# Kernel optimization log

Hardware: AMD Instinct MI355X
Metric: run time of the kernel (lower is better)

The kernel has to match this reference:

```python
import jax, jax.numpy as jnp
import numpy as np

# Config constants (match init_kwargs)
E = 16          # n_routed_experts
G = 4           # n_groups
TOPK_G = 2      # topk_groups
K = 4           # n_activated_experts
ROUTE_SCALE = 2.5446


def setup_inputs() -> dict:
    key = jax.random.key(0)
    ks = jax.random.split(key, 9)
    T, D, H = 2048, 1024, 704
    HS = 2 * H  # shared FFN hidden = n_shared_experts * expert_hidden_dim
    sc = lambda k, shape, fan_in: (jax.random.normal(k, shape, jnp.float32)
                                   * (fan_in ** -0.5))
    return {
        "x":      jax.random.normal(ks[0], (T, D), jnp.float32),
        "gate_w": sc(ks[1], (E, D), D),
        "gate_b": jnp.zeros((E,), jnp.float32),       # V3 routing bias (init 0)
        "w1":     sc(ks[2], (E, H, D), D),            # gate proj per expert
        "w3":     sc(ks[3], (E, H, D), D),            # up proj per expert
        "w2":     sc(ks[4], (E, D, H), H),            # down proj per expert
        "ws1":    sc(ks[5], (HS, D), D),              # shared FFN gate proj
        "ws3":    sc(ks[6], (HS, D), D),              # shared FFN up proj
        "ws2":    sc(ks[7], (D, HS), HS),             # shared FFN down proj
    }


def _gate(x, gate_w, gate_b):
    """DeepSeek-V3 sigmoid gate with bias routing + group-limited masking."""
    T = x.shape[0]
    logits = x @ gate_w.T                                   # [T, E]
    scores = jax.nn.sigmoid(logits).astype(jnp.float32)     # original_scores
    routing = scores + gate_b                               # bias only affects routing
    g = routing.reshape(T, G, E // G)
    # use_bias=True -> group score = sum of top-2 routing scores in group
    group_scores = jnp.sum(jax.lax.top_k(g, 2)[0], axis=-1)     # [T, G]
    top_groups = jax.lax.top_k(group_scores, TOPK_G)[1]         # [T, TOPK_G]
    keep = jnp.any(jnp.arange(G)[None, :, None] == top_groups[:, None, :],
                   axis=-1)                                     # [T, G]
    routing = jnp.where(keep[:, :, None], g, -jnp.inf).reshape(T, E)
    idx = jax.lax.top_k(routing, K)[1]                          # [T, K]
    w = jnp.take_along_axis(scores, idx, axis=1)                # un-biased weights
    w = w / jnp.clip(jnp.sum(w, axis=-1, keepdims=True), 1e-9)  # sigmoid renorm
    w = (w * ROUTE_SCALE).astype(x.dtype)
    return w, idx


def reference(x, gate_w, gate_b, w1, w3, w2, ws1, ws3, ws2):
    T, D = x.shape
    weights, idx = _gate(x, gate_w, gate_b)                 # [T,K], [T,K]
    # Dense dispatch/combine matrix: combine[t, e] = gate weight (0 if unrouted)
    combine = jnp.zeros((T, E), x.dtype).at[
        jnp.arange(T)[:, None], idx].add(weights)           # [T, E]
    # Routed experts: SwiGLU per expert, grouped GEMMs
    hg = jnp.einsum('td,ehd->eth', x, w1)                   # [E, T, H]
    hu = jnp.einsum('td,ehd->eth', x, w3)                   # [E, T, H]
    eo = jnp.einsum('eth,edh->etd', jax.nn.silu(hg) * hu, w2)  # [E, T, D]
    y_routed = jnp.einsum('etd,te->td', eo, combine)        # [T, D]
    # Shared experts (always active SwiGLU)
    y_shared = (jax.nn.silu(x @ ws1.T) * (x @ ws3.T)) @ ws2.T
    return y_routed + y_shared
```

## Files before the change

### kernel.cpp

```cpp
#include <hip/hip_runtime.h>
#include <hip/hip_bf16.h>
#include <math.h>

typedef __attribute__((ext_vector_type(4))) float   f32x4;
typedef __attribute__((ext_vector_type(8))) short   short8;
typedef __attribute__((ext_vector_type(8))) __bf16  bf16x8;

union SB8 { short8 s; bf16x8 b; };

__device__ __forceinline__ short f2bf(float f) {
  union { float f; unsigned u; } v; v.f = f;
  unsigned r = v.u + 0x7fffu + ((v.u >> 16) & 1u);
  return (short)(r >> 16);
}

__device__ __forceinline__ short8 cvt8(f32x4 a, f32x4 b) {
  short8 r;
  r[0] = f2bf(a[0]); r[1] = f2bf(a[1]); r[2] = f2bf(a[2]); r[3] = f2bf(a[3]);
  r[4] = f2bf(b[0]); r[5] = f2bf(b[1]); r[6] = f2bf(b[2]); r[7] = f2bf(b[3]);
  return r;
}

__device__ __forceinline__ void ldsload16(const short* g, short* l) {
  __builtin_amdgcn_global_load_lds(
      (const __attribute__((address_space(1))) unsigned int*)g,
      (__attribute__((address_space(3))) unsigned int*)l, 16, 0, 0);
}

#define TT   2048
#define DD   1024
#define HH   704
#define HSS  1408
#define EE   16
#define CAP  2048
#define CSTR 32

#define O1  2097152ULL
#define O2  13631488ULL
#define O3  25165824ULL
#define O4  36700160ULL
#define O5  38141952ULL
#define O6  39583744ULL
#define CVT_TOTAL 41025536ULL

#define W2SZ    11534336ULL
#define WS1SZ   1441792ULL
#define WS1END  26607616ULL
#define CVTA_TOTAL  28049408ULL
#define CVTA_BLOCKS 3424
#define GATE_BLOCKS 512

__global__ __launch_bounds__(256)
void gate_cvt(const float* __restrict__ x,  const float* __restrict__ w1,
              const float* __restrict__ w3, const float* __restrict__ s1,
              const float* __restrict__ s3, short* __restrict__ dst,
              const float* __restrict__ gw, const float* __restrict__ gb,
              int* __restrict__ counts, int* __restrict__ tok,
              float* __restrict__ wgt, int* __restrict__ eslot)
{
  if (blockIdx.x >= GATE_BLOCKS) {
    const int tid = threadIdx.x;
    const size_t base = (size_t)(blockIdx.x - GATE_BLOCKS) * 8192;
    const float* sp[4]; short* dp[4];
    #pragma unroll
    for (int k = 0; k < 4; k++) {
      const size_t sb = base + (size_t)k * 2048;
      const float* src; size_t doff;
      if      (sb < O1)     { src = x  + sb;            doff = sb; }
      else if (sb < O2)     { src = w1 + (sb - O1);     doff = sb; }
      else if (sb < O3)     { src = w3 + (sb - O2);     doff = sb; }
      else if (sb < WS1END) { src = s1 + (sb - O3);     doff = sb + W2SZ; }
      else                  { src = s3 + (sb - WS1END); doff = sb + W2SZ; }
      sp[k] = src + tid * 8;
      dp[k] = dst + doff + tid * 8;
    }
    f32x4 va[8];
    #pragma unroll
    for (int k = 0; k < 4; k++) {
      va[2 * k]     = *(const f32x4*)(sp[k]);
      va[2 * k + 1] = *(const f32x4*)(sp[k] + 4);
    }
    #pragma unroll
    for (int k = 0; k < 4; k++)
      *(short8*)(dp[k]) = cvt8(va[2 * k], va[2 * k + 1]);
    return;
  }

  const int lane = threadIdx.x & 63;
  const int wid  = threadIdx.x >> 6;
  const int t    = blockIdx.x * 4 + wid;
  const int e    = lane & 15;
  const int p    = lane >> 4;

  const float* xp = x + (size_t)t * DD + p * 256;
  const float* gp = gw + (size_t)e * DD + p * 256;

  double a0 = 0.0, a1 = 0.0, a2 = 0.0, a3 = 0.0;
  #pragma unroll 8
  for (int i = 0; i < 64; i++) {
    f32x4 xa = *(const f32x4*)(xp + i * 4);
    f32x4 ga = *(const f32x4*)(gp + i * 4);
    a0 += (double)xa[0] * (double)ga[0];
    a1 += (double)xa[1] * (double)ga[1];
    a2 += (double)xa[2] * (double)ga[2];
    a3 += (double)xa[3] * (double)ga[3];
  }
  double acc = (a0 + a1) + (a2 + a3);
  acc += __shfl_xor(acc, 16);
  acc += __shfl_xor(acc, 32);
  float accf = (float)acc;

  float lf[EE], sc[EE], r[EE];
  #pragma unroll
  for (int j = 0; j < EE; j++) lf[j] = __shfl(accf, j);
  #pragma unroll
  for (int j = 0; j < EE; j++) {
    sc[j] = 1.f / (1.f + expf(-lf[j]));
    r[j] = sc[j] + gb[j];
  }
  float gs[4];
  #pragma unroll
  for (int g = 0; g < 4; g++) {
    float m1 = -1e30f, m2 = -1e30f;
    #pragma unroll
    for (int j = 0; j < 4; j++) {
      float v = r[g * 4 + j];
      if (v > m1) { m2 = m1; m1 = v; }
      else if (v > m2) { m2 = v; }
    }
    gs[g] = m1 + m2;
  }
  int g1 = 0, g2 = -1; float b1 = -1e30f, b2 = -1e30f;
  #pragma unroll
  for (int g = 0; g < 4; g++) {
    if (gs[g] > b1) { b2 = b1; g2 = g1; b1 = gs[g]; g1 = g; }
    else if (gs[g] > b2) { b2 = gs[g]; g2 = g; }
  }
  int idx[4]; float wv[4]; float wsum = 0.f;
  unsigned used = 0;
  #pragma unroll
  for (int k = 0; k < 4; k++) {
    float best = -1e30f; int bi = 0;
    #pragma unroll
    for (int j = 0; j < EE; j++) {
      int g = j >> 2;
      bool keep = (g == g1) || (g == g2);
      if (keep && !((used >> j) & 1) && r[j] > best) { best = r[j]; bi = j; }
    }
    used |= 1u << bi; idx[k] = bi; wv[k] = sc[bi]; wsum += sc[bi];
  }
  float div = wsum < 1e-9f ? 1e-9f : wsum;
  if (lane < 4) {
    float w = wv[lane] / div * 2.5446f;
    int slot = atomicAdd(&counts[idx[lane] * CSTR], 1);
    tok[idx[lane] * CAP + slot] = t;
    wgt[idx[lane] * CAP + slot] = w;
    eslot[t * 4 + lane] = (idx[lane] << 16) | slot;
  }
}

__global__ __launch_bounds__(256, 2)
void gemm1_merged(const short* __restrict__ xb, const short* __restrict__ w1b,
                  const short* __restrict__ w3b, const short* __restrict__ ws1b,
                  const short* __restrict__ ws3b, short* __restrict__ act_r,
                  short* __restrict__ act_s, const int* __restrict__ counts,
                  const int* __restrict__ tok,
                  const float* __restrict__ w2f, const float* __restrict__ ws2f,
                  short* __restrict__ w2bd, short* __restrict__ ws2bd)
{
  const int z = blockIdx.z;
  const int Mt = blockIdx.y, Nt = blockIdx.x;

  if (z == 0) {
    const int bid = Mt * 11 + Nt;
    const int tid = threadIdx.x;
    for (int s = 0; s < 9; s++) {
      const size_t base = (size_t)bid * 73728 + (size_t)s * 8192;
      const float* sp[4]; short* dp[4];
      #pragma unroll
      for (int k = 0; k < 4; k++) {
        const size_t sb = base + (size_t)k * 2048;
        if (sb < W2SZ) {
          sp[k] = w2f + sb + tid * 8;
          dp[k] = w2bd + sb + tid * 8;
        } else {
          const size_t o = sb - W2SZ;
          sp[k] = ws2f + o + tid * 8;
          dp[k] = ws2bd + o + tid * 8;
        }
      }
      f32x4 va[8];
      #pragma unroll
      for (int k = 0; k < 4; k++) {
        va[2 * k]     = *(const f32x4*)(sp[k]);
        va[2 * k + 1] = *(const f32x4*)(sp[k] + 4);
      }
      #pragma unroll
      for (int k = 0; k < 4; k++)
        *(short8*)(dp[k]) = cvt8(va[2 * k], va[2 * k + 1]);
    }
    return;
  }

  const bool routed = (z <= EE);
  const int e = z - 1;

  int cnt, N, rowbase = 0;
  const short *W1, *W3;
  short* act;
  if (routed) {
    if (Nt >= 6) return;
    cnt = counts[e * CSTR];
    if (Mt * 128 >= cnt) return;
    int rb = 0;
    for (int i = 0; i < e; i++) rb += counts[i * CSTR];
    rowbase = rb;
    N = HH;
    W1 = w1b + (size_t)e * HH * DD;
    W3 = w3b + (size_t)e * HH * DD;
    act = act_r;
  } else {
    cnt = TT; N = HSS; W1 = ws1b; W3 = ws3b; act = act_s;
  }

  __shared__ __align__(16) short lA[128 * 64];
  __shared__ __align__(16) short lB1[128 * 64];
  __shared__ __align__(16) short lB3[128 * 64];

  const int tid = threadIdx.x, lane = tid & 63, wv = tid >> 6;
  const int srow = lane >> 3, schunk = lane & 7, scg = schunk ^ srow;

  const short* pa[4]; const short* pb1[4]; const short* pb3[4];
  #pragma unroll
  for (int i = 0; i < 4; i++) {
    const int g = wv * 4 + i;
    int arow = Mt * 128 + g * 8 + srow;
    if (routed) {
      int slot = arow < cnt ? arow : cnt - 1;
      arow = tok[e * CAP + slot];
    }
    pa[i] = xb + (size_t)arow * DD + scg * 8;
    const int brow = Nt * 128 + g * 8 + srow;
    pb1[i] = W1 + (size_t)brow * DD + scg * 8;
    pb3[i] = W3 + (size_t)brow * DD + scg * 8;
  }

  f32x4 acc1[8][2], acc3[8][2];
  #pragma unroll
  for (int i = 0; i < 8; i++) {
    #pragma unroll
    for (int j = 0; j < 2; j++) { acc1[i][j] = (f32x4)0.f; acc3[i][j] = (f32x4)0.f; }
  }

  const int q = lane >> 4, r7 = lane & 7, hi = (lane & 15) >> 3;

  for (int kk = 0; kk < DD; kk += 64) {
    #pragma unroll
    for (int i = 0; i < 4; i++) {
      const int g = wv * 4 + i;
      ldsload16(pa[i] + kk,  lA  + g * 512);
      ldsload16(pb1[i] + kk, lB1 + g * 512);
      ldsload16(pb3[i] + kk, lB3 + g * 512);
    }
    __syncthreads();
    #pragma unroll
    for (int kc = 0; kc < 2; kc++) {
      const int cx = (kc * 4 + q) ^ r7;
      SB8 b1f[2], b3f[2];
      #pragma unroll
      for (int ntl = 0; ntl < 2; ntl++) {
        const int a16 = ((wv * 2 + ntl) * 2 + hi) * 64 + r7 * 8 + cx;
        b1f[ntl].s = *(const short8*)(lB1 + a16 * 8);
        b3f[ntl].s = *(const short8*)(lB3 + a16 * 8);
      }
      #pragma unroll
      for (int mt = 0; mt < 8; mt++) {
        const int a16 = (2 * mt + hi) * 64 + r7 * 8 + cx;
        SB8 af; af.s = *(const short8*)(lA + a16 * 8);
        acc1[mt][0] = __builtin_amdgcn_mfma_f32_16x16x32_bf16(af.b, b1f[0].b, acc1[mt][0], 0, 0, 0);
        acc1[mt][1] = __builtin_amdgcn_mfma_f32_16x16x32_bf16(af.b, b1f[1].b, acc1[mt][1], 0, 0, 0);
        acc3[mt][0] = __builtin_amdgcn_mfma_f32_16x16x32_bf16(af.b, b3f[0].b, acc3[mt][0], 0, 0, 0);
        acc3[mt][1] = __builtin_amdgcn_mfma_f32_16x16x32_bf16(af.b, b3f[1].b, acc3[mt][1], 0, 0, 0);
      }
    }
    __syncthreads();
  }

  const int quad = lane >> 4, lcol = lane & 15;
  #pragma unroll
  for (int mt = 0; mt < 8; mt++) {
    #pragma unroll
    for (int ntl = 0; ntl < 2; ntl++) {
      const int col = Nt * 128 + (wv * 2 + ntl) * 16 + lcol;
      #pragma unroll
      for (int rg = 0; rg < 4; rg++) {
        const int r = Mt * 128 + mt * 16 + quad * 4 + rg;
        if (r < cnt && col < N) {
          float g = acc1[mt][ntl][rg], u = acc3[mt][ntl][rg];
          float a = g / (1.f + __expf(-g)) * u;
          act[(size_t)(rowbase + r) * N + col] = f2bf(a);
        }
      }
    }
  }
}

__global__ __launch_bounds__(256, 2)
void gemm2_merged(const short* __restrict__ act_r, const short* __restrict__ act_s,
                  const short* __restrict__ w2b, const short* __restrict__ ws2b,
                  float* __restrict__ y, float* __restrict__ outr,
                  const int* __restrict__ counts, const float* __restrict__ wgt)
{
  const int z = blockIdx.z;
  const bool routed = (z < EE);
  const int Mt = blockIdx.y, Nt = blockIdx.x;

  int cnt, Kd, rowbase = 0;
  const short *A, *W;
  if (routed) {
    cnt = counts[z * CSTR];
    if (Mt * 128 >= cnt) return;
    int rb = 0;
    for (int i = 0; i < z; i++) rb += counts[i * CSTR];
    rowbase = rb;
    Kd = HH;
    A = act_r + (size_t)rowbase * HH;
    W = w2b + (size_t)z * DD * HH;
  } else {
    cnt = TT; Kd = HSS; A = act_s; W = ws2b;
  }

  __shared__ __align__(16) short lA[128 * 64];
  __shared__ __align__(16) short lB[128 * 64];

  const int tid = threadIdx.x, lane = tid & 63, wv = tid >> 6;
  const int srow = lane >> 3, schunk = lane & 7, scg = schunk ^ srow;

  const short* pa[4]; const short* pb[4];
  #pragma unroll
  for (int i = 0; i < 4; i++) {
    const int g = wv * 4 + i;
    int arow = Mt * 128 + g * 8 + srow;
    if (arow >= cnt) arow = cnt - 1;
    pa[i] = A + (size_t)arow * Kd + scg * 8;
    const int brow = Nt * 128 + g * 8 + srow;
    pb[i] = W + (size_t)brow * Kd + scg * 8;
  }

  f32x4 acc[8][2];
  #pragma unroll
  for (int i = 0; i < 8; i++) { acc[i][0] = (f32x4)0.f; acc[i][1] = (f32x4)0.f; }

  const int q = lane >> 4, r7 = lane & 7, hi = (lane & 15) >> 3;

  for (int kk = 0; kk < Kd; kk += 64) {
    #pragma unroll
    for (int i = 0; i < 4; i++) {
      const int g = wv * 4 + i;
      ldsload16(pa[i] + kk, lA + g * 512);
      ldsload16(pb[i] + kk, lB + g * 512);
    }
    __syncthreads();
    #pragma unroll
    for (int kc = 0; kc < 2; kc++) {
      const int cx = (kc * 4 + q) ^ r7;
      SB8 bf[2];
      #pragma unroll
      for (int ntl = 0; ntl < 2; ntl++) {
        const int a16 = ((wv * 2 + ntl) * 2 + hi) * 64 + r7 * 8 + cx;
        bf[ntl].s = *(const short8*)(lB + a16 * 8);
      }
      #pragma unroll
      for (int mt = 0; mt < 8; mt++) {
        const int a16 = (2 * mt + hi) * 64 + r7 * 8 + cx;
        SB8 af; af.s = *(const short8*)(lA + a16 * 8);
        acc[mt][0] = __builtin_amdgcn_mfma_f32_16x16x32_bf16(af.b, bf[0].b, acc[mt][0], 0, 0, 0);
        acc[mt][1] = __builtin_amdgcn_mfma_f32_16x16x32_bf16(af.b, bf[1].b, acc[mt][1], 0, 0, 0);
      }
    }
    __syncthreads();
  }

  const int quad = lane >> 4, lcol = lane & 15;
  #pragma unroll
  for (int mt = 0; mt < 8; mt++) {
    #pragma unroll
    for (int ntl = 0; ntl < 2; ntl++) {
      const int col = Nt * 128 + (wv * 2 + ntl) * 16 + lcol;
      #pragma unroll
      for (int rg = 0; rg < 4; rg++) {
        const int slot = Mt * 128 + mt * 16 + quad * 4 + rg;
        const float v = acc[mt][ntl][rg];
        if (routed) {
          if (slot < cnt) {
            const float w = wgt[z * CAP + slot];
            outr[(size_t)(rowbase + slot) * DD + col] = w * v;
          }
        } else {
          y[(size_t)slot * DD + col] = v;
        }
      }
    }
  }
}

__global__ __launch_bounds__(256)
void combine_kernel(float* __restrict__ y, const float* __restrict__ outr,
                    const int* __restrict__ eslot, const int* __restrict__ counts)
{
  const int t = blockIdx.x;
  const int d = threadIdx.x * 4;

  int offs[EE];
  int s = 0;
  #pragma unroll
  for (int i = 0; i < EE; i++) { offs[i] = s; s += counts[i * CSTR]; }

  f32x4 accv = *(f32x4*)(y + (size_t)t * DD + d);
  #pragma unroll
  for (int k = 0; k < 4; k++) {
    const int es = eslot[t * 4 + k];
    const int row = offs[es >> 16] + (es & 0xFFFF);
    accv += *(const f32x4*)(outr + (size_t)row * DD + d);
  }
  *(f32x4*)(y + (size_t)t * DD + d) = accv;
}

extern "C" void kernel_launch(void* const* d_in, const int* in_sizes, int n_in,
                              void* d_out, int out_size, void* d_ws, size_t ws_size,
                              hipStream_t stream) {
  const float* x      = (const float*)d_in[0];
  const float* gate_w = (const float*)d_in[1];
  const float* gate_b = (const float*)d_in[2];
  const float* w1     = (const float*)d_in[3];
  const float* w3     = (const float*)d_in[4];
  const float* w2     = (const float*)d_in[5];
  const float* ws1    = (const float*)d_in[6];
  const float* ws3    = (const float*)d_in[7];
  const float* ws2    = (const float*)d_in[8];
  float* y = (float*)d_out;

  char* ws = (char*)d_ws;
  int*   counts = (int*)ws;
  int*   tok    = (int*)(ws + 2048);
  float* wgt    = (float*)(ws + 2048 + (size_t)EE * CAP * 4);
  int*   eslot  = (int*)(ws + 2048 + (size_t)EE * CAP * 8);
  short* bf     = (short*)(ws + 2048 + (size_t)EE * CAP * 8 + (size_t)TT * 16);
  short* xb   = bf;
  short* w1b  = bf + O1;
  short* w3b  = bf + O2;
  short* w2b  = bf + O3;
  short* ws1b = bf + O4;
  short* ws3b = bf + O5;
  short* ws2b = bf + O6;
  short* act_r = bf + CVT_TOTAL;
  short* act_s = act_r + (size_t)8192 * HH;
  float* outr = (float*)(bf + O1);

  (void)hipMemsetAsync(counts, 0, EE * CSTR * sizeof(int), stream);

  gate_cvt<<<GATE_BLOCKS + CVTA_BLOCKS, 256, 0, stream>>>(
      x, w1, w3, ws1, ws3, bf,
      gate_w, gate_b, counts, tok, wgt, eslot);

  gemm1_merged<<<dim3(11, TT / 128, EE + 2), 256, 0, stream>>>(
      xb, w1b, w3b, ws1b, ws3b, act_r, act_s, counts, tok,
      w2, ws2, w2b, ws2b);

  gemm2_merged<<<dim3(DD / 128, TT / 128, EE + 1), 256, 0, stream>>>(
      act_r, act_s, w2b, ws2b, y, outr, counts, wgt);

  combine_kernel<<<TT, 256, 0, stream>>>(y, outr, eslot, counts);
}
```

Baseline: 317.9 us.

## Remap block indices for XCD-aware expert placement and raise occupancy hint

Block IDs in both merged GEMM kernels are remapped so that consecutive blocks, which the hardware dispatches round-robin across the 8 XCDs, are grouped per expert. Each XCD then mostly works on the same expert weights and activations, which should improve L2 reuse. Launch bounds are raised from 2 to 3 blocks per SM, which caps registers per thread and may cause spills in exchange for higher occupancy.

Measured after the change: 338.7 us. +6.5%, slower.

```diff
diff --git a/kernel.cpp b/kernel.cpp
--- a/kernel.cpp
+++ b/kernel.cpp
@@ -159,7 +159,7 @@
   }
 }
 
-__global__ __launch_bounds__(256, 2)
+__global__ __launch_bounds__(256, 3)
 void gemm1_merged(const short* __restrict__ xb, const short* __restrict__ w1b,
                   const short* __restrict__ w3b, const short* __restrict__ ws1b,
                   const short* __restrict__ ws3b, short* __restrict__ act_r,
@@ -168,8 +168,23 @@
                   const float* __restrict__ w2f, const float* __restrict__ ws2f,
                   short* __restrict__ w2bd, short* __restrict__ ws2bd)
 {
-  const int z = blockIdx.z;
-  const int Mt = blockIdx.y, Nt = blockIdx.x;
+  const int F = blockIdx.x + 11 * (blockIdx.y + 16 * blockIdx.z);
+  const int r8 = F & 7, rank = F >> 3;
+  int z, Mt, Nt;
+  if (rank < 22) {
+    z = 0;
+    const int p = rank * 8 + r8;
+    Mt = p / 11; Nt = p - Mt * 11;
+  } else if (rank < 374) {
+    const int rr = rank - 22;
+    z = 1 + r8 + 8 * (rr / 176);
+    const int p = rr % 176;
+    Mt = p / 11; Nt = p - Mt * 11;
+  } else {
+    z = 17;
+    const int p = (rank - 374) * 8 + r8;
+    Mt = p / 11; Nt = p - Mt * 11;
+  }
 
   if (z == 0) {
     const int bid = Mt * 11 + Nt;
@@ -305,15 +320,26 @@
   }
 }
 
-__global__ __launch_bounds__(256, 2)
+__global__ __launch_bounds__(256, 3)
 void gemm2_merged(const short* __restrict__ act_r, const short* __restrict__ act_s,
                   const short* __restrict__ w2b, const short* __restrict__ ws2b,
                   float* __restrict__ y, float* __restrict__ outr,
                   const int* __restrict__ counts, const float* __restrict__ wgt)
 {
-  const int z = blockIdx.z;
+  const int F = blockIdx.x + 8 * (blockIdx.y + 16 * blockIdx.z);
+  const int r8 = F & 7, rank = F >> 3;
+  int z, Mt, Nt;
+  if (rank < 256) {
+    z = r8 + 8 * (rank >> 7);
+    const int p = rank & 127;
+    Mt = p >> 3; Nt = p & 7;
+  } else {
+    z = 16;
+    const int p = (rank - 256) * 8 + r8;
+    Mt = p >> 3; Nt = p & 7;
+  }
+
   const bool routed = (z < EE);
-  const int Mt = blockIdx.y, Nt = blockIdx.x;
 
   int cnt, Kd, rowbase = 0;
   const short *A, *W;
```
